# Kernel optimization log

Hardware: AMD Instinct MI355X
Metric: run time of the kernel (lower is better)

The kernel has to match this reference:

```python
import jax, jax.numpy as jnp
import numpy as np

LOSS_WEIGHT = 1.0
INTENSITY_WEIGHT = 0.5


def setup_inputs() -> dict:
    key = jax.random.key(0)
    k1, k2 = jax.random.split(key)
    N = 8192
    adv_pc = jax.random.normal(k1, (N, 4), dtype=jnp.float32)
    ori_pc = jax.random.normal(k2, (N, 4), dtype=jnp.float32)
    return {"adv_pc": adv_pc, "ori_pc": ori_pc}


def reference(adv_pc, ori_pc):
    # Scale the intensity channel (index 3) by intensity_weight, as in forward().
    scale = jnp.array([1.0, 1.0, 1.0, INTENSITY_WEIGHT], dtype=adv_pc.dtype)
    a = adv_pc * scale  # [N, 4]
    b = ori_pc * scale  # [M, 4]
    # knn_points with K=1 returns SQUARED euclidean distance to nearest neighbor.
    # Use the ||a||^2 + ||b||^2 - 2 a.b expansion to avoid an [N, M, 4] diff tensor.
    a2 = jnp.sum(a * a, axis=-1)          # [N]
    b2 = jnp.sum(b * b, axis=-1)          # [M]
    cross = jnp.einsum('nd,md->nm', a, b)  # [N, M]
    sqdist = a2[:, None] + b2[None, :] - 2.0 * cross  # [N, M]
    min_d = jnp.min(sqdist, axis=-1)      # per-adv-point nearest sq distance, [N]
    hd = jnp.max(min_d)                   # one-sided Hausdorff (squared)
    # original keeps the batch dim of size 1 after max(-1)
    return jnp.reshape(hd * LOSS_WEIGHT, (1,))
```

## Files before the change

kernel.cpp:

```cpp
#include <hip/hip_runtime.h>
#include <math.h>

#define THREADS 256
#define APT 8
#define TILE 64

__global__ __launch_bounds__(THREADS) void hd_partial_min(
    const float* __restrict__ adv, const float* __restrict__ ori,
    float* __restrict__ ws,
    int N, int M, int N_pad, int chunks)
{
    __shared__ float4 sb[TILE];
    __shared__ float  sb2[TILE];

    const int tid = threadIdx.x;
    const int base_i = blockIdx.x * (THREADS * APT) + tid;

    float4 a[APT];
    #pragma unroll
    for (int k = 0; k < APT; ++k) {
        int i = base_i + k * THREADS;
        float4 v = make_float4(0.f, 0.f, 0.f, 0.f);
        if (i < N) v = ((const float4*)adv)[i];
        a[k].x = -2.0f * v.x;
        a[k].y = -2.0f * v.y;
        a[k].z = -2.0f * v.z;
        a[k].w = -v.w;
    }

    float m[APT];
    #pragma unroll
    for (int k = 0; k < APT; ++k) m[k] = INFINITY;

    for (int base = blockIdx.y * TILE; base < M; base += chunks * TILE) {
        for (int k = tid; k < TILE; k += THREADS) {
            int j = base + k;
            float4 b = make_float4(0.f, 0.f, 0.f, 0.f);
            float b2 = INFINITY;
            if (j < M) {
                b = ((const float4*)ori)[j];
                b.w *= 0.5f;
                b2 = b.x*b.x + b.y*b.y + b.z*b.z + b.w*b.w;
            }
            sb[k]  = b;
            sb2[k] = b2;
        }
        __syncthreads();

        for (int j = 0; j < TILE; j += 4) {
            float4 p0 = sb[j+0], p1 = sb[j+1], p2 = sb[j+2], p3 = sb[j+3];
            float4 q  = ((const float4*)sb2)[j >> 2];
            #pragma unroll
            for (int k = 0; k < APT; ++k) {
                float ax = a[k].x, ay = a[k].y, az = a[k].z, aw = a[k].w;
                float d0 = fmaf(ax, p0.x, fmaf(ay, p0.y, fmaf(az, p0.z, fmaf(aw, p0.w, q.x))));
                float d1 = fmaf(ax, p1.x, fmaf(ay, p1.y, fmaf(az, p1.z, fmaf(aw, p1.w, q.y))));
                float d2 = fmaf(ax, p2.x, fmaf(ay, p2.y, fmaf(az, p2.z, fmaf(aw, p2.w, q.z))));
                float d3 = fmaf(ax, p3.x, fmaf(ay, p3.y, fmaf(az, p3.z, fmaf(aw, p3.w, q.w))));
                m[k] = fminf(fminf(m[k], d0), fminf(d1, fminf(d2, d3)));
            }
        }
        __syncthreads();
    }

    #pragma unroll
    for (int k = 0; k < APT; ++k) {
        int i = base_i + k * THREADS;
        if (i < N) {
            float aa = a[k].x*a[k].x + a[k].y*a[k].y + a[k].z*a[k].z + a[k].w*a[k].w;
            float d  = fmaf(0.25f, aa, m[k]);
            ws[(size_t)blockIdx.y * N_pad + i] = fmaxf(d, 0.0f);
        }
    }
}

__global__ __launch_bounds__(THREADS) void hd_reduce(
    const float* __restrict__ ws, float* __restrict__ out,
    int N, int N_pad, int rows)
{
    int i = blockIdx.x * THREADS + threadIdx.x;
    float m = 0.0f;
    if (i < N) {
        float mm[8];
        #pragma unroll
        for (int u = 0; u < 8; ++u) mm[u] = INFINITY;
        int r = 0;
        for (; r + 7 < rows; r += 8) {
            #pragma unroll
            for (int u = 0; u < 8; ++u)
                mm[u] = fminf(mm[u], ws[(size_t)(r + u) * N_pad + i]);
        }
        for (; r < rows; ++r)
            mm[0] = fminf(mm[0], ws[(size_t)r * N_pad + i]);
        m = fminf(fminf(fminf(mm[0], mm[1]), fminf(mm[2], mm[3])),
                  fminf(fminf(mm[4], mm[5]), fminf(mm[6], mm[7])));
    }
    for (int off = 32; off >= 1; off >>= 1)
        m = fmaxf(m, __shfl_down(m, off, 64));
    __shared__ float smax[THREADS / 64];
    int lane = threadIdx.x & 63, wave = threadIdx.x >> 6;
    if (lane == 0) smax[wave] = m;
    __syncthreads();
    if (threadIdx.x == 0) {
        float bm = smax[0];
        #pragma unroll
        for (int w = 1; w < THREADS / 64; ++w) bm = fmaxf(bm, smax[w]);
        atomicMax((int*)out, __float_as_int(bm));
    }
}

extern "C" void kernel_launch(void* const* d_in, const int* in_sizes, int n_in,
                              void* d_out, int out_size, void* d_ws, size_t ws_size,
                              hipStream_t stream) {
    const float* adv = (const float*)d_in[0];
    const float* ori = (const float*)d_in[1];
    float* out = (float*)d_out;
    float* ws  = (float*)d_ws;

    int N = in_sizes[0] / 4;
    int M = in_sizes[1] / 4;

    int gx    = (N + THREADS * APT - 1) / (THREADS * APT);
    int N_pad = gx * THREADS * APT;

    int chunks = (M + TILE - 1) / TILE;
    if (chunks > 128) chunks = 128;
    while (chunks > 1 && (size_t)chunks * (size_t)N_pad * sizeof(float) > ws_size)
        chunks >>= 1;

    hd_partial_min<<<dim3(gx, chunks), THREADS, 0, stream>>>(
        adv, ori, ws, N, M, N_pad, chunks);
    hd_reduce<<<(N + THREADS - 1) / THREADS, THREADS, 0, stream>>>(
        ws, out, N, N_pad, chunks);
}
```

Baseline: 71.35 us.

## Replace partial-min workspace with per-point atomicMin and single-block final max

Instead of writing a chunks-by-N workspace of partial minima and reducing it in a second wide kernel, each block now atomically mins its per-point result into a single N-length int array initialised by a memset, and one 1024-thread block computes the final max. Points per thread drop from 8 to 4 and the chunk count is retuned to target about 512 blocks, to raise parallelism. This removes the large workspace traffic but adds a memset launch, atomic contention, and a serial single-block tail. The int-bit atomicMin relies on all values being non-negative floats.

```diff
diff --git a/kernel.cpp b/kernel.cpp
--- a/kernel.cpp
+++ b/kernel.cpp
@@ -2,16 +2,17 @@
 #include <math.h>
 
 #define THREADS 256
-#define APT 8
+#define APT 4
 #define TILE 64
+#define RTHREADS 1024
 
-__global__ __launch_bounds__(THREADS) void hd_partial_min(
+__global__ __launch_bounds__(THREADS) void hd_min_atomic(
     const float* __restrict__ adv, const float* __restrict__ ori,
-    float* __restrict__ ws,
-    int N, int M, int N_pad, int chunks)
+    int* __restrict__ mins,
+    int N, int M, int chunks)
 {
     __shared__ float4 sb[TILE];
-    __shared__ float  sb2[TILE];
+    __shared__ __align__(16) float sb2[TILE];
 
     const int tid = threadIdx.x;
     const int base_i = blockIdx.x * (THREADS * APT) + tid;
@@ -47,6 +48,7 @@
         }
         __syncthreads();
 
+        #pragma unroll 4
         for (int j = 0; j < TILE; j += 4) {
             float4 p0 = sb[j+0], p1 = sb[j+1], p2 = sb[j+2], p3 = sb[j+3];
             float4 q  = ((const float4*)sb2)[j >> 2];
@@ -57,7 +59,7 @@
                 float d1 = fmaf(ax, p1.x, fmaf(ay, p1.y, fmaf(az, p1.z, fmaf(aw, p1.w, q.y))));
                 float d2 = fmaf(ax, p2.x, fmaf(ay, p2.y, fmaf(az, p2.z, fmaf(aw, p2.w, q.z))));
                 float d3 = fmaf(ax, p3.x, fmaf(ay, p3.y, fmaf(az, p3.z, fmaf(aw, p3.w, q.w))));
-                m[k] = fminf(fminf(m[k], d0), fminf(d1, fminf(d2, d3)));
+                m[k] = fminf(m[k], fminf(fminf(d0, d1), fminf(d2, d3)));
             }
         }
         __syncthreads();
@@ -68,44 +70,29 @@
         int i = base_i + k * THREADS;
         if (i < N) {
             float aa = a[k].x*a[k].x + a[k].y*a[k].y + a[k].z*a[k].z + a[k].w*a[k].w;
-            float d  = fmaf(0.25f, aa, m[k]);
-            ws[(size_t)blockIdx.y * N_pad + i] = fmaxf(d, 0.0f);
+            float d  = fmaxf(fmaf(0.25f, aa, m[k]), 0.0f);
+            atomicMin(&mins[i], __float_as_int(d));
         }
     }
 }
 
-__global__ __launch_bounds__(THREADS) void hd_reduce(
-    const float* __restrict__ ws, float* __restrict__ out,
-    int N, int N_pad, int rows)
+__global__ __launch_bounds__(RTHREADS) void hd_final_max(
+    const int* __restrict__ mins, float* __restrict__ out, int N)
 {
-    int i = blockIdx.x * THREADS + threadIdx.x;
     float m = 0.0f;
-    if (i < N) {
-        float mm[8];
-        #pragma unroll
-        for (int u = 0; u < 8; ++u) mm[u] = INFINITY;
-        int r = 0;
-        for (; r + 7 < rows; r += 8) {
-            #pragma unroll
-            for (int u = 0; u < 8; ++u)
-                mm[u] = fminf(mm[u], ws[(size_t)(r + u) * N_pad + i]);
-        }
-        for (; r < rows; ++r)
-            mm[0] = fminf(mm[0], ws[(size_t)r * N_pad + i]);
-        m = fminf(fminf(fminf(mm[0], mm[1]), fminf(mm[2], mm[3])),
-                  fminf(fminf(mm[4], mm[5]), fminf(mm[6], mm[7])));
-    }
+    for (int i = threadIdx.x; i < N; i += RTHREADS)
+        m = fmaxf(m, __int_as_float(mins[i]));
     for (int off = 32; off >= 1; off >>= 1)
         m = fmaxf(m, __shfl_down(m, off, 64));
-    __shared__ float smax[THREADS / 64];
+    __shared__ float smax[RTHREADS / 64];
     int lane = threadIdx.x & 63, wave = threadIdx.x >> 6;
     if (lane == 0) smax[wave] = m;
     __syncthreads();
     if (threadIdx.x == 0) {
         float bm = smax[0];
         #pragma unroll
-        for (int w = 1; w < THREADS / 64; ++w) bm = fmaxf(bm, smax[w]);
-        atomicMax((int*)out, __float_as_int(bm));
+        for (int w = 1; w < RTHREADS / 64; ++w) bm = fmaxf(bm, smax[w]);
+        out[0] = bm;
     }
 }
 
@@ -115,7 +102,7 @@
     const float* adv = (const float*)d_in[0];
     const float* ori = (const float*)d_in[1];
     float* out = (float*)d_out;
-    float* ws  = (float*)d_ws;
+    int*   mins = (int*)d_ws;
 
     int N = in_sizes[0] / 4;
     int M = in_sizes[1] / 4;
@@ -123,13 +110,14 @@
     int gx    = (N + THREADS * APT - 1) / (THREADS * APT);
     int N_pad = gx * THREADS * APT;
 
-    int chunks = (M + TILE - 1) / TILE;
-    if (chunks > 128) chunks = 128;
-    while (chunks > 1 && (size_t)chunks * (size_t)N_pad * sizeof(float) > ws_size)
-        chunks >>= 1;
+    int maxtiles = (M + TILE - 1) / TILE;
+    int chunks = 512 / gx;
+    if (chunks < 1) chunks = 1;
+    if (chunks > maxtiles) chunks = maxtiles;
 
-    hd_partial_min<<<dim3(gx, chunks), THREADS, 0, stream>>>(
-        adv, ori, ws, N, M, N_pad, chunks);
-    hd_reduce<<<(N + THREADS - 1) / THREADS, THREADS, 0, stream>>>(
-        ws, out, N, N_pad, chunks);
+    hipMemsetAsync(mins, 0x7F, (size_t)N_pad * sizeof(int), stream);
+
+    hd_min_atomic<<<dim3(gx, chunks), THREADS, 0, stream>>>(
+        adv, ori, mins, N, M, chunks);
+    hd_final_max<<<1, RTHREADS, 0, stream>>>(mins, out, N);
 }
```

New measurement: 68.10 us. 1.05x faster.
